# Optimization experiments

Hardware: AMD Instinct MI355X
Metric: run time of the kernel (lower is better)

## Reference

```python
import jax, jax.numpy as jnp
import numpy as np

EPS = 1e-6
RATIO = 0.5


def lrelu(x):
    return jnp.where(x > 0, x, 0.1 * x)


def conv1x1(x, w, b):
    # x (B,Ci,H,W), w (Co,Ci)
    return jnp.einsum('bihw,oi->bohw', x, w) + b[None, :, None, None]


def conv3x3(x, w, b, groups=1):
    y = jax.lax.conv_general_dilated(x, w, (1, 1), [(1, 1), (1, 1)],
        dimension_numbers=('NCHW', 'OIHW', 'NCHW'), feature_group_count=groups)
    return y + b[None, :, None, None]


def ln_cf(x, w, b):
    # channels-first LayerNorm over dim 1 (matches custom LayerNorm in source)
    u = x.mean(1, keepdims=True)
    s = ((x - u) ** 2).mean(1, keepdims=True)
    xn = (x - u) / jnp.sqrt(s + EPS)
    return w[None, :, None, None] * xn + b[None, :, None, None]


def flow_warp(x, flow):
    # bilinear warp, align_corners=True, zeros padding; flow (B,H,W,2): ch0=col offset, ch1=row offset (pixels)
    B, C, H, W = x.shape
    sx = jnp.arange(W, dtype=x.dtype)[None, None, :] + flow[..., 0]
    sy = jnp.arange(H, dtype=x.dtype)[None, :, None] + flow[..., 1]
    x0 = jnp.floor(sx)
    y0 = jnp.floor(sy)
    flat = x.reshape(B, C, H * W)

    def gather(xi, yi):
        valid = ((xi >= 0) & (xi <= W - 1) & (yi >= 0) & (yi <= H - 1)).astype(x.dtype)
        xc = jnp.clip(xi, 0, W - 1).astype(jnp.int32)
        yc = jnp.clip(yi, 0, H - 1).astype(jnp.int32)
        idx = (yc * W + xc).reshape(B, H * W)
        g = jnp.take_along_axis(flat, idx[:, None, :], axis=2).reshape(B, C, H, W)
        return g * valid[:, None, :, :]

    wx = sx - x0
    wy = sy - y0
    return (gather(x0, y0) * ((1 - wx) * (1 - wy))[:, None]
            + gather(x0 + 1, y0) * (wx * (1 - wy))[:, None]
            + gather(x0, y0 + 1) * ((1 - wx) * wy)[:, None]
            + gather(x0 + 1, y0 + 1) * (wx * wy)[:, None])


def mixer_forward(x, p_in_w, p_in_b, p_ln_w, p_ln_b, p_off_w1, p_off_b1, p_off_w2, p_off_b2,
                  p_ca_w, p_ca_b, p_sa_w, p_sa_b, p_mask_w1, p_mask_b1, p_mask_w2, p_mask_b2,
                  v_w, v_b, q_w, q_b, k_w, k_b, cs_w, cs_b, out_w, out_b):
    B, C, H, W = x.shape
    N = H * W
    # ---- Predictor (eval path) ----
    gy, gx = jnp.meshgrid(jnp.linspace(-1.0, 1.0, H), jnp.linspace(-1.0, 1.0, W), indexing='ij')
    grid = jnp.broadcast_to(jnp.stack([gx, gy]).astype(x.dtype)[None], (B, 2, H, W))
    cond = jnp.concatenate([x, grid], axis=1)  # (B, C+2, H, W)
    f = lrelu(ln_cf(conv1x1(cond, p_in_w, p_in_b), p_ln_w, p_ln_b))  # (B, (C+2)//4, H, W)
    offsets = jnp.tanh(conv1x1(lrelu(conv1x1(f, p_off_w1, p_off_b1)), p_off_w2, p_off_b2)) * 8.0
    ca = jax.nn.sigmoid(conv1x1(f.mean((2, 3), keepdims=True), p_ca_w, p_ca_b))  # (B,C,1,1)
    sa = jax.nn.sigmoid(conv3x3(f, p_sa_w, p_sa_b))  # (B,1,H,W)
    t = f.mean(1).reshape(B, N, 1)  # window_size=1 -> per-pixel token score input
    s1 = lrelu(t @ p_mask_w1.T + p_mask_b1)
    pred = jax.nn.softmax(s1 @ p_mask_w2.T + p_mask_b2, axis=-1)  # (B,N,2)
    score = pred[..., 0]
    num_keep = int(N * RATIO)  # static keep count (eval-mode deterministic routing)
    idx = jnp.argsort(-score, axis=1)
    idx1, idx2 = idx[:, :num_keep], idx[:, num_keep:]
    # ---- routed mixing ----
    v = conv1x1(x, v_w, v_b)
    k_img = x + flow_warp(x, offsets.transpose(0, 2, 3, 1))
    tok = lambda z: z.reshape(B, C, N).transpose(0, 2, 1)
    q_tok, k_tok, v_tok, vs_tok = tok(x), tok(k_img), tok(v), tok(v * sa)
    sel = lambda z, i: jnp.take_along_axis(z, i[..., None], axis=1)
    q1 = sel(q_tok, idx1) @ q_w.T + q_b
    k1 = sel(k_tok, idx1) @ k_w.T + k_b
    v1 = sel(v_tok, idx1)
    attn = jax.nn.softmax(jnp.einsum('bnc,bmc->bnm', q1, k1) * (C ** -0.5), axis=-1)
    f_attn = jnp.einsum('bnm,bmc->bnc', attn, v1)
    bi = jnp.arange(B)[:, None]
    out_tok = v_tok.at[bi, idx1].set(f_attn).at[bi, idx2].set(sel(vs_tok, idx2))  # batch_index_fill
    out = out_tok.transpose(0, 2, 1).reshape(B, C, H, W)
    out = jax.nn.gelu(conv3x3(out, cs_w, cs_b, groups=C)) * ca + out
    return conv1x1(out, out_w, out_b)


def setup_inputs():
    key = jax.random.key(0)
    ks = iter(jax.random.split(key, 40))
    B, C, H, W = 8, 192, 64, 64
    CD, C4, C8 = C + 2, (C + 2) // 4, (C + 2) // 8

    def w(shape, fan):
        return jax.random.normal(next(ks), shape, jnp.float32) * (fan ** -0.5)

    return dict(
        x=jax.random.normal(next(ks), (B, C, H, W), jnp.float32),
        p_in_w=w((C4, CD), CD), p_in_b=jnp.zeros((C4,)),
        p_ln_w=jnp.ones((C4,)), p_ln_b=jnp.zeros((C4,)),
        p_off_w1=w((C8, C4), C4), p_off_b1=jnp.zeros((C8,)),
        p_off_w2=w((2, C8), C8), p_off_b2=jnp.zeros((2,)),
        p_ca_w=w((C, C4), C4), p_ca_b=jnp.zeros((C,)),
        p_sa_w=w((1, C4, 3, 3), C4 * 9), p_sa_b=jnp.zeros((1,)),
        p_mask_w1=w((1, 1), 1), p_mask_b1=jnp.zeros((1,)),
        p_mask_w2=w((2, 1), 1), p_mask_b2=jnp.zeros((2,)),
        v_w=w((C, C), C), v_b=jnp.zeros((C,)),
        q_w=w((C, C), C), q_b=jnp.zeros((C,)),
        k_w=w((C, C), C), k_b=jnp.zeros((C,)),
        cs_w=w((C, 1, 3, 3), 9), cs_b=jnp.zeros((C,)),
        out_w=w((C, C), C), out_b=jnp.zeros((C,)),
    )


def reference(x, p_in_w, p_in_b, p_ln_w, p_ln_b, p_off_w1, p_off_b1, p_off_w2, p_off_b2,
              p_ca_w, p_ca_b, p_sa_w, p_sa_b, p_mask_w1, p_mask_b1, p_mask_w2, p_mask_b2,
              v_w, v_b, q_w, q_b, k_w, k_b, cs_w, cs_b, out_w, out_b):
    return mixer_forward(x, p_in_w, p_in_b, p_ln_w, p_ln_b, p_off_w1, p_off_b1, p_off_w2, p_off_b2,
                         p_ca_w, p_ca_b, p_sa_w, p_sa_b, p_mask_w1, p_mask_b1, p_mask_w2, p_mask_b2,
                         v_w, v_b, q_w, q_b, k_w, k_b, cs_w, cs_b, out_w, out_b)
```

## Files before the change

### kernel.cpp

```cpp
#include <hip/hip_runtime.h>
#include <hip/hip_bf16.h>

#define NB   8
#define NC   192
#define NH   64
#define NW   64
#define NN   4096
#define NCD  194
#define NC4  48
#define NKEEP 2048
#define NSPLIT 4
#define KPS   (NKEEP/NSPLIT)
#define NT    (KPS/32)

typedef __attribute__((ext_vector_type(8))) short bf16x8;
typedef __attribute__((ext_vector_type(4))) float f32x4;
typedef __hip_bfloat16 bf16;

__device__ __forceinline__ float dsigmoid(float x){ return 1.f/(1.f+__expf(-x)); }
__device__ __forceinline__ float dlrelu(float x){ return x>0.f ? x : 0.1f*x; }
__device__ __forceinline__ float b2f(short s){ return __uint_as_float(((unsigned)(unsigned short)s)<<16); }

__global__ __launch_bounds__(128) void k_f_score(
    const float* __restrict__ x, const float* __restrict__ w_in, const float* __restrict__ b_in,
    const float* __restrict__ ln_w, const float* __restrict__ ln_b,
    const float* __restrict__ mw1, const float* __restrict__ mb1,
    const float* __restrict__ mw2, const float* __restrict__ mb2,
    float* __restrict__ f, float* __restrict__ score)
{
  __shared__ float wT[NCD][NC4];
  int t = threadIdx.x;
  for (int i=t; i<NCD*NC4; i+=128){ int o = i/NCD, c = i - o*NCD; wT[c][o] = w_in[i]; }
  __syncthreads();

  int gid = blockIdx.x*128 + t;
  int p = gid & (NN-1), b = gid >> 12;
  int hh = p>>6, ww = p&63;

  f32x4 a4[12];
  #pragma unroll
  for (int j=0;j<12;++j) a4[j] = *(const f32x4*)(b_in + 4*j);

  const float* xb = x + (size_t)b*NC*NN + p;
  for (int c=0;c<NC;++c){
    float xv = xb[(size_t)c*NN];
    #pragma unroll
    for (int j=0;j<12;++j){ f32x4 wv = *(const f32x4*)&wT[c][4*j]; a4[j] += wv*xv; }
  }
  { float gx = -1.f + (2.f/63.f)*(float)ww;
    #pragma unroll
    for (int j=0;j<12;++j){ f32x4 wv = *(const f32x4*)&wT[192][4*j]; a4[j] += wv*gx; }
    float gy = -1.f + (2.f/63.f)*(float)hh;
    #pragma unroll
    for (int j=0;j<12;++j){ f32x4 wv = *(const f32x4*)&wT[193][4*j]; a4[j] += wv*gy; }
  }
  float s1=0.f, s2=0.f;
  #pragma unroll
  for (int j=0;j<12;++j){
    #pragma unroll
    for (int k=0;k<4;++k){ float v=a4[j][k]; s1+=v; s2+=v*v; }
  }
  float mean = s1*(1.f/NC4);
  float var  = s2*(1.f/NC4) - mean*mean;
  float rstd = rsqrtf(var + 1e-6f);
  float tsum = 0.f;
  #pragma unroll
  for (int j=0;j<12;++j){
    f32x4 lw = *(const f32x4*)(ln_w + 4*j);
    f32x4 lb = *(const f32x4*)(ln_b + 4*j);
    #pragma unroll
    for (int k=0;k<4;++k){
      float z = lw[k]*((a4[j][k]-mean)*rstd) + lb[k];
      float fv = z>0.f ? z : 0.1f*z;
      tsum += fv;
      f[((size_t)b*NC4 + 4*j+k)*NN + p] = fv;
    }
  }
  float tm = tsum*(1.f/NC4);
  float sv = dlrelu(tm*mw1[0] + mb1[0]);
  float d  = sv*(mw2[0]-mw2[1]) + (mb2[0]-mb2[1]);
  score[b*NN + p] = dsigmoid(d);
}

__global__ __launch_bounds__(1024) void k_topk(const float* __restrict__ score,
                                               int* __restrict__ idx1, int* __restrict__ flag)
{
  int b = blockIdx.x;
  int t = threadIdx.x;
  __shared__ unsigned hist[256];
  __shared__ unsigned long long sP;
  __shared__ unsigned sR;
  __shared__ unsigned cnt;
  unsigned long long key[4];
  #pragma unroll
  for (int j=0;j<4;++j){
    int i = t + j*1024;
    unsigned u = __float_as_uint(score[b*NN+i]);
    unsigned a = (u & 0x80000000u) ? ~u : (u | 0x80000000u);
    unsigned d = ~a;
    key[j] = ((unsigned long long)d << 32) | (unsigned)i;
  }
  if (t==0){ sP=0ull; sR=NKEEP-1; cnt=0u; }
  #pragma unroll 1
  for (int pass=0; pass<8; ++pass){
    int shift = 56 - pass*8;
    if (t<256) hist[t]=0u;
    __syncthreads();
    unsigned long long P = sP;
    #pragma unroll
    for (int j=0;j<4;++j){
      bool ok = (pass==0) || ((key[j] >> (shift+8)) == (P >> (shift+8)));
      if (ok) atomicAdd(&hist[(unsigned)((key[j]>>shift)&255ull)], 1u);
    }
    __syncthreads();
    if (t < 64){
      unsigned s[4]; unsigned lsum=0u;
      #pragma unroll
      for (int j=0;j<4;++j){ s[j]=hist[4*t+j]; lsum+=s[j]; }
      unsigned incl = lsum;
      #pragma unroll
      for (int d2=1; d2<64; d2<<=1){
        unsigned v = __shfl_up(incl, d2);
        if (t >= d2) incl += v;
      }
      unsigned before = incl - lsum;
      unsigned R = sR;
      if (R >= before && R < incl){
        unsigned c = before;
        #pragma unroll
        for (int j=0;j<4;++j){
          if (R < c + s[j]){
            sP = sP | ((unsigned long long)(4u*(unsigned)t + (unsigned)j) << shift);
            sR = R - c;
            break;
          }
          c += s[j];
        }
      }
    }
    __syncthreads();
  }
  unsigned long long P = sP;
  #pragma unroll
  for (int j=0;j<4;++j){
    int i = t + j*1024;
    bool sel = (key[j] <= P);
    flag[b*NN+i] = sel ? 1 : 0;
    if (sel){
      unsigned pos = atomicAdd(&cnt, 1u);
      idx1[b*NKEEP + pos] = i;
    }
  }
}

__global__ __launch_bounds__(256) void k_offsets(
    const float* __restrict__ f, const float* __restrict__ w1, const float* __restrict__ b1,
    const float* __restrict__ w2, const float* __restrict__ b2, float* __restrict__ offs)
{
  int gid = blockIdx.x*256 + threadIdx.x;
  int p = gid & (NN-1);
  int b = gid >> 12;
  const float* fb = f + (size_t)b*NC4*NN + p;
  float fl[NC4];
  #pragma unroll 8
  for (int c=0;c<NC4;++c) fl[c] = fb[(size_t)c*NN];
  float h1[24];
  for (int o=0;o<24;++o){
    const float* wr = w1 + o*NC4;
    float a = b1[o];
    #pragma unroll 8
    for (int c=0;c<NC4;++c) a += wr[c]*fl[c];
    h1[o] = dlrelu(a);
  }
  #pragma unroll
  for (int o=0;o<2;++o){
    const float* wr = w2 + o*24;
    float a = b2[o];
    #pragma unroll
    for (int c=0;c<24;++c) a += wr[c]*h1[c];
    offs[((size_t)b*2+o)*NN + p] = tanhf(a)*8.f;
  }
}

__global__ __launch_bounds__(256) void k_fmean(const float* __restrict__ f, float* __restrict__ fmean){
  int bc = blockIdx.x;
  const float* p = f + (size_t)bc*NN;
  float s = 0.f;
  for (int i=threadIdx.x;i<NN;i+=256) s += p[i];
  for (int o=32;o;o>>=1) s += __shfl_xor(s,o);
  __shared__ float r[4];
  if ((threadIdx.x&63)==0) r[threadIdx.x>>6] = s;
  __syncthreads();
  if (threadIdx.x==0) fmean[bc] = (r[0]+r[1]+r[2]+r[3])*(1.f/NN);
}

__global__ void k_ca(const float* __restrict__ fmean, const float* __restrict__ w,
                     const float* __restrict__ bias, float* __restrict__ ca){
  int b = blockIdx.x, o = threadIdx.x;
  const float* fm = fmean + b*NC4;
  float a = bias[o];
  #pragma unroll 8
  for (int c=0;c<NC4;++c) a += w[o*NC4+c]*fm[c];
  ca[b*NC+o] = dsigmoid(a);
}

__global__ __launch_bounds__(256) void k_sa(const float* __restrict__ f, const float* __restrict__ w,
                                            const float* __restrict__ bias, float* __restrict__ sa){
  int hh = blockIdx.x;
  int b  = blockIdx.y;
  __shared__ float fl[3][NC4][66];
  __shared__ float wl[NC4*9];
  __shared__ float ps[4][64];
  int t = threadIdx.x;

  for (int i=t; i<3*NC4*64; i+=256){
    int col = i & 63;
    int rc  = i >> 6;
    int cc  = rc % NC4;
    int rr  = rc / NC4;
    int yy  = hh + rr - 1;
    float v = (yy>=0 && yy<=63) ? f[((size_t)b*NC4+cc)*NN + yy*64 + col] : 0.f;
    fl[rr][cc][1+col] = v;
  }
  if (t < 3*NC4){ int rr=t/NC4, cc=t%NC4; fl[rr][cc][0]=0.f; fl[rr][cc][65]=0.f; }
  for (int i=t; i<NC4*9; i+=256) wl[i] = w[i];
  __syncthreads();

  int ww = t & 63, gq = t >> 6;
  float acc = 0.f;
  #pragma unroll
  for (int j=0;j<12;++j){
    int cc = gq*12 + j;
    const float* wc = &wl[cc*9];
    #pragma unroll
    for (int dy=0;dy<3;++dy){
      acc += fl[dy][cc][ww  ]*wc[dy*3+0];
      acc += fl[dy][cc][ww+1]*wc[dy*3+1];
      acc += fl[dy][cc][ww+2]*wc[dy*3+2];
    }
  }
  ps[gq][ww] = acc;
  __syncthreads();
  if (t < 64){
    float s = ps[0][t]+ps[1][t]+ps[2][t]+ps[3][t] + bias[0];
    sa[(size_t)b*NN + hh*64 + t] = dsigmoid(s);
  }
}

__global__ __launch_bounds__(256) void k_w2bf(const float* __restrict__ a, const float* __restrict__ b,
                                              const float* __restrict__ c, const float* __restrict__ d,
                                              bf16* __restrict__ oa, bf16* __restrict__ ob,
                                              bf16* __restrict__ oc, bf16* __restrict__ od){
  int i = blockIdx.x*256 + threadIdx.x;
  if (i < NC*NC){
    oa[i] = __float2bfloat16(a[i]);
    ob[i] = __float2bfloat16(b[i]);
    oc[i] = __float2bfloat16(c[i]);
    od[i] = __float2bfloat16(d[i]);
  }
}

__global__ __launch_bounds__(256) void k_transpose(const float* __restrict__ in, bf16* __restrict__ outT){
  int b = blockIdx.z;
  int c0 = blockIdx.y*32, p0 = blockIdx.x*32;
  __shared__ float tile[32][33];
  int col = threadIdx.x & 31, row8 = threadIdx.x >> 5;
  #pragma unroll
  for (int ph=0;ph<4;++ph){
    int c = c0 + ph*8 + row8;
    tile[ph*8+row8][col] = in[((size_t)b*NC + c)*NN + p0 + col];
  }
  __syncthreads();
  #pragma unroll
  for (int ph=0;ph<4;++ph){
    int p = p0 + ph*8 + row8;
    outT[((size_t)b*NN + p)*NC + c0 + col] = __float2bfloat16(tile[col][ph*8+row8]);
  }
}

__global__ __launch_bounds__(256) void k_conv_mfma(const bf16* __restrict__ inT, const bf16* __restrict__ wb,
                                                   const float* __restrict__ bias, float* __restrict__ outp){
  int b = blockIdx.y;
  int px0 = blockIdx.x*64;
  int wv = threadIdx.x>>6, lane = threadIdx.x&63, g = lane>>4, r = lane&15;
  int o0 = wv*48;
  bf16x8 bw[3][6];
  #pragma unroll
  for (int jo=0;jo<3;++jo)
    #pragma unroll
    for (int ks=0;ks<6;++ks)
      bw[jo][ks] = *(const bf16x8*)(wb + (size_t)(o0+jo*16+r)*NC + ks*32 + 8*g);
  float bv[3];
  #pragma unroll
  for (int jo=0;jo<3;++jo) bv[jo] = bias[o0+jo*16+r];

  const bf16* ib = inT + (size_t)b*NN*NC;
  #pragma unroll
  for (int t=0;t<4;++t){
    int px = px0 + t*16;
    bf16x8 a[6];
    #pragma unroll
    for (int ks=0;ks<6;++ks) a[ks] = *(const bf16x8*)(ib + (size_t)(px+r)*NC + ks*32 + 8*g);
    f32x4 acc[3];
    #pragma unroll
    for (int jo=0;jo<3;++jo){ acc[jo][0]=0.f; acc[jo][1]=0.f; acc[jo][2]=0.f; acc[jo][3]=0.f; }
    #pragma unroll
    for (int ks=0;ks<6;++ks)
      #pragma unroll
      for (int jo=0;jo<3;++jo)
        acc[jo] = __builtin_amdgcn_mfma_f32_16x16x32_bf16(a[ks], bw[jo][ks], acc[jo], 0,0,0);
    #pragma unroll
    for (int jo=0;jo<3;++jo){
      float4 rv; rv.x=acc[jo][0]+bv[jo]; rv.y=acc[jo][1]+bv[jo]; rv.z=acc[jo][2]+bv[jo]; rv.w=acc[jo][3]+bv[jo];
      *(float4*)(outp + ((size_t)b*NC + o0+jo*16+r)*NN + px + 4*g) = rv;
    }
  }
}

__global__ __launch_bounds__(256) void k_gemm_mfma(const bf16* __restrict__ in, const bf16* __restrict__ wb,
                                                   const float* __restrict__ bias, bf16* __restrict__ outp){
  int b = blockIdx.y;
  int s0 = blockIdx.x*32;
  int wv = threadIdx.x>>6, lane = threadIdx.x&63, g = lane>>4, r = lane&15;
  int o0 = wv*48;
  bf16x8 bw[3][6];
  #pragma unroll
  for (int jo=0;jo<3;++jo)
    #pragma unroll
    for (int ks=0;ks<6;++ks)
      bw[jo][ks] = *(const bf16x8*)(wb + (size_t)(o0+jo*16+r)*NC + ks*32 + 8*g);
  float bv[3];
  #pragma unroll
  for (int jo=0;jo<3;++jo) bv[jo] = bias[o0+jo*16+r];

  const bf16* ib = in + (size_t)b*NKEEP*NC;
  bf16* ob = outp + (size_t)b*NKEEP*NC;
  #pragma unroll
  for (int t=0;t<2;++t){
    int s = s0 + t*16;
    bf16x8 a[6];
    #pragma unroll
    for (int ks=0;ks<6;++ks) a[ks] = *(const bf16x8*)(ib + (size_t)(s+r)*NC + ks*32 + 8*g);
    f32x4 acc[3];
    #pragma unroll
    for (int jo=0;jo<3;++jo){ acc[jo][0]=0.f; acc[jo][1]=0.f; acc[jo][2]=0.f; acc[jo][3]=0.f; }
    #pragma unroll
    for (int ks=0;ks<6;++ks)
      #pragma unroll
      for (int jo=0;jo<3;++jo)
        acc[jo] = __builtin_amdgcn_mfma_f32_16x16x32_bf16(a[ks], bw[jo][ks], acc[jo], 0,0,0);
    #pragma unroll
    for (int jo=0;jo<3;++jo)
      #pragma unroll
      for (int i=0;i<4;++i)
        ob[(size_t)(s+4*g+i)*NC + o0+jo*16+r] = __float2bfloat16(acc[jo][i]+bv[jo]);
  }
}

__global__ __launch_bounds__(256) void k_warp_params(const int* __restrict__ idx1, const float* __restrict__ offs,
                                                     float4* __restrict__ wpar, int4* __restrict__ ipar){
  int gid = blockIdx.x*256 + threadIdx.x;
  int b = gid >> 11;
  int p = idx1[gid];
  int ph = p >> 6, pwx = p & 63;
  float fx = offs[((size_t)b*2+0)*NN + p];
  float fy = offs[((size_t)b*2+1)*NN + p];
  float sx = (float)pwx + fx, sy = (float)ph + fy;
  float x0f = floorf(sx), y0f = floorf(sy);
  float wx = sx - x0f, wy = sy - y0f;
  int x0 = (int)x0f, y0 = (int)y0f;
  bool vx0 = (x0f >= 0.f) && (x0f <= 63.f);
  bool vx1 = (x0f+1.f >= 0.f) && (x0f+1.f <= 63.f);
  bool vy0 = (y0f >= 0.f) && (y0f <= 63.f);
  bool vy1 = (y0f+1.f >= 0.f) && (y0f+1.f <= 63.f);
  int cx0 = min(max(x0,0),63), cx1 = min(max(x0+1,0),63);
  int cy0 = min(max(y0,0),63), cy1 = min(max(y0+1,0),63);
  float4 w4;
  w4.x = (vx0&&vy0) ? (1.f-wx)*(1.f-wy) : 0.f;
  w4.y = (vx1&&vy0) ? wx*(1.f-wy)       : 0.f;
  w4.z = (vx0&&vy1) ? (1.f-wx)*wy       : 0.f;
  w4.w = (vx1&&vy1) ? wx*wy             : 0.f;
  int4 i4;
  i4.x = cy0*64+cx0; i4.y = cy0*64+cx1; i4.z = cy1*64+cx0; i4.w = cy1*64+cx1;
  wpar[gid]=w4; ipar[gid]=i4;
}

__global__ __launch_bounds__(256) void k_gather_qT(const bf16* __restrict__ xT, const int* __restrict__ idx1,
                                                   bf16* __restrict__ qin){
  int gid = blockIdx.x*256 + threadIdx.x;
  int j = gid % 24;
  int bs = gid / 24;
  int b = bs >> 11;
  int p = idx1[bs];
  *(bf16x8*)(qin + (size_t)bs*NC + j*8) = *(const bf16x8*)(xT + ((size_t)b*NN + p)*NC + j*8);
}

__global__ __launch_bounds__(256) void k_gather_kT(const bf16* __restrict__ xT, const int* __restrict__ idx1,
                                                   const float4* __restrict__ wpar, const int4* __restrict__ ipar,
                                                   bf16* __restrict__ kin){
  int gid = blockIdx.x*256 + threadIdx.x;
  int j = gid % 24;
  int bs = gid / 24;
  int b = bs >> 11;
  int p = idx1[bs];
  float4 w4 = wpar[bs]; int4 i4 = ipar[bs];
  const bf16* xb = xT + (size_t)b*NN*NC + j*8;
  bf16x8 v0 = *(const bf16x8*)(xb + (size_t)p*NC);
  bf16x8 v1 = *(const bf16x8*)(xb + (size_t)i4.x*NC);
  bf16x8 v2 = *(const bf16x8*)(xb + (size_t)i4.y*NC);
  bf16x8 v3 = *(const bf16x8*)(xb + (size_t)i4.z*NC);
  bf16x8 v4 = *(const bf16x8*)(xb + (size_t)i4.w*NC);
  bf16x8 o;
  #pragma unroll
  for (int k=0;k<8;++k){
    float vv = b2f(v0[k]) + w4.x*b2f(v1[k]) + w4.y*b2f(v2[k]) + w4.z*b2f(v3[k]) + w4.w*b2f(v4[k]);
    bf16 h = __float2bfloat16(vv);
    o[k] = *(short*)&h;
  }
  *(bf16x8*)(kin + (size_t)bs*NC + j*8) = o;
}

__global__ __launch_bounds__(256) void k_gather_vT(const float* __restrict__ v, const int* __restrict__ idx1,
                                                   bf16* __restrict__ v1T){
  int gid = blockIdx.x*256 + threadIdx.x;
  int s = gid & (NKEEP-1);
  int bc = gid >> 11;
  int b = bc/NC;
  v1T[gid] = __float2bfloat16(v[(size_t)bc*NN + idx1[b*NKEEP+s]]);
}

__global__ __launch_bounds__(256) void k_fill(const float* __restrict__ sa, const int* __restrict__ flag,
                                              float* __restrict__ vout){
  int gid = blockIdx.x*256 + threadIdx.x;
  int p = gid & (NN-1);
  int bc = gid >> 12;
  int b = bc/NC;
  if (!flag[b*NN+p]) vout[gid] *= sa[b*NN+p];
}

__global__ __launch_bounds__(256) void k_attn(const bf16* __restrict__ q1, const bf16* __restrict__ k1,
                                              const bf16* __restrict__ v1T,
                                              bf16* __restrict__ pacc, float* __restrict__ pl)
{
  int b = blockIdx.y, qb = blockIdx.x, sp = blockIdx.z;
  int tid = threadIdx.x;
  int wv = tid >> 6;
  int lane = tid & 63;
  int g = lane >> 4, r = lane & 15;
  int q0 = qb*64 + wv*16;

  const bf16* qbp = q1 + (size_t)b*NKEEP*NC;
  const char* kgb = (const char*)(k1 + (size_t)b*NKEEP*NC);
  const char* vgb = (const char*)(v1T + (size_t)b*NC*NKEEP);

  __shared__ __align__(1024) char kl[12288];
  __shared__ __align__(1024) char vl[2][12288];
  __shared__ __align__(16) bf16 plds[4][16][40];
  bf16 (* __restrict__ pw)[40] = plds[wv];
  char* klc = kl;

  int ksrc[3], vsrc[3];
  #pragma unroll
  for (int i=0;i<3;++i){
    int j = wv*3 + i;
    int o = j*1024 + lane*16;
    int rr = o/384, cb = o - rr*384;
    ksrc[i] = rr*384 + (cb ^ ((rr&7)<<4));
    int ch = o>>6, kb2 = o&63;
    vsrc[i] = ch*(NKEEP*2) + kb2;
  }

  const int kbase = sp*KPS;
  auto stage = [&](int k0, int vb){
    char* vlc = vl[vb];
    #pragma unroll
    for (int i=0;i<3;++i){
      int j = wv*3 + i;
      __builtin_amdgcn_global_load_lds(
        (const __attribute__((address_space(1))) void*)(kgb + (size_t)k0*384 + ksrc[i]),
        (__attribute__((address_space(3))) void*)(klc + j*1024), 16, 0, 0);
      __builtin_amdgcn_global_load_lds(
        (const __attribute__((address_space(1))) void*)(vgb + (size_t)k0*2 + vsrc[i]),
        (__attribute__((address_space(3))) void*)(vlc + j*1024), 16, 0, 0);
    }
  };

  bf16x8 aq[6];
  #pragma unroll
  for (int ks=0;ks<6;++ks)
    aq[ks] = *(const bf16x8*)(qbp + (size_t)(q0+r)*NC + 32*ks + 8*g);

  f32x4 acc[12];
  #pragma unroll
  for (int i=0;i<12;++i){ acc[i][0]=0.f; acc[i][1]=0.f; acc[i][2]=0.f; acc[i][3]=0.f; }
  float l[4]={0.f,0.f,0.f,0.f};

  const float scale = 0.07216878364870323f;
  const float shift = 20.f;
  const int swz = (r&7)<<4;

  stage(kbase, 0);
  __syncthreads();

  int vb = 0;
  for (int t16=0;t16<NT;++t16) {
    f32x4 s0v, s1v;
    s0v[0]=s0v[1]=s0v[2]=s0v[3]=0.f;
    s1v[0]=s1v[1]=s1v[2]=s1v[3]=0.f;
    #pragma unroll
    for (int ks=0;ks<6;++ks) {
      int co = (ks*64 + g*16) ^ swz;
      bf16x8 bk0 = *(const bf16x8*)(klc + r*384 + co);
      bf16x8 bk1 = *(const bf16x8*)(klc + (16+r)*384 + co);
      s0v = __builtin_amdgcn_mfma_f32_16x16x32_bf16(aq[ks], bk0, s0v, 0,0,0);
      s1v = __builtin_amdgcn_mfma_f32_16x16x32_bf16(aq[ks], bk1, s1v, 0,0,0);
    }
    #pragma unroll
    for (int i=0;i<4;++i) {
      float e0 = __expf(s0v[i]*scale - shift);
      float e1 = __expf(s1v[i]*scale - shift);
      l[i] += e0 + e1;
      pw[4*g+i][r]    = __float2bfloat16(e0);
      pw[4*g+i][16+r] = __float2bfloat16(e1);
    }
    bf16x8 pa = *(const bf16x8*)(&pw[r][8*g]);

    __syncthreads();
    if (t16+1 < NT) stage(kbase + (t16+1)*32, vb^1);

    const char* vlc = vl[vb];
    #pragma unroll
    for (int ct=0;ct<12;++ct) {
      bf16x8 bvv = *(const bf16x8*)(vlc + (16*ct + r)*64 + g*16);
      acc[ct] = __builtin_amdgcn_mfma_f32_16x16x32_bf16(pa, bvv, acc[ct], 0,0,0);
    }
    __syncthreads();
    vb ^= 1;
  }

  #pragma unroll
  for (int i=0;i<4;++i){
    #pragma unroll
    for (int o=1;o<16;o<<=1) l[i] += __shfl_xor(l[i],o);
  }
  size_t pbase = (((size_t)(b*32+qb)*NSPLIT + sp)*64);
  if (r==0){
    #pragma unroll
    for (int i=0;i<4;++i) pl[pbase + wv*16 + 4*g + i] = l[i];
  }
  #pragma unroll
  for (int ct=0;ct<12;++ct)
    #pragma unroll
    for (int i=0;i<4;++i)
      pacc[(pbase + wv*16 + 4*g + i)*NC + 16*ct + r] = __float2bfloat16(acc[ct][i]);
}

__global__ __launch_bounds__(256) void k_merge(const bf16* __restrict__ pacc,
                                               const float* __restrict__ pl, const int* __restrict__ idx1,
                                               float* __restrict__ out_img)
{
  int gid = blockIdx.x*256 + threadIdx.x;
  int c = gid % NC;
  int bs = gid / NC;
  int s = bs & (NKEEP-1);
  int b = bs >> 11;
  int qb = s >> 6, ql = s & 63;
  size_t base = ((size_t)(b*32+qb)*NSPLIT)*64 + ql;
  float l = pl[base] + pl[base+64] + pl[base+128] + pl[base+192];
  size_t pb = base*NC + c;
  float v = __bfloat162float(pacc[pb])
          + __bfloat162float(pacc[pb + (size_t)64*NC])
          + __bfloat162float(pacc[pb + (size_t)128*NC])
          + __bfloat162float(pacc[pb + (size_t)192*NC]);
  out_img[((size_t)b*NC + c)*NN + idx1[b*NKEEP + s]] = v / l;
}

__global__ __launch_bounds__(256) void k_dwgelu(const float* __restrict__ vin, const float* __restrict__ ca,
                                                const float* __restrict__ cw, const float* __restrict__ cb,
                                                float* __restrict__ out2){
  int bc = blockIdx.x;
  int c = bc % NC, b = bc / NC;
  __shared__ float tl[66][66];
  int t = threadIdx.x;

  if (t < 66){ tl[0][t] = 0.f; tl[65][t] = 0.f; }
  if (t < 64){ tl[t+1][0] = 0.f; tl[t+1][65] = 0.f; }
  const float* ip = vin + (size_t)bc*NN;
  #pragma unroll
  for (int k=0;k<4;++k){
    int p4 = (t + k*256)*4;
    int hh = p4 >> 6, ww = p4 & 63;
    float4 v4 = *(const float4*)(ip + p4);
    tl[1+hh][1+ww  ] = v4.x;
    tl[1+hh][1+ww+1] = v4.y;
    tl[1+hh][1+ww+2] = v4.z;
    tl[1+hh][1+ww+3] = v4.w;
  }
  float wr[9];
  #pragma unroll
  for (int i=0;i<9;++i) wr[i] = cw[c*9+i];
  float cbv = cb[c];
  float cav = ca[b*NC+c];
  __syncthreads();

  float* op = out2 + (size_t)bc*NN;
  #pragma unroll
  for (int k=0;k<16;++k){
    int p = t + k*256;
    int hh = p >> 6, ww = p & 63;
    float a = cbv;
    #pragma unroll
    for (int dy=0;dy<3;++dy){
      a += tl[hh+dy][ww  ]*wr[dy*3+0];
      a += tl[hh+dy][ww+1]*wr[dy*3+1];
      a += tl[hh+dy][ww+2]*wr[dy*3+2];
    }
    float gl = 0.5f*a*(1.f+tanhf(0.79788456080286536f*(a+0.044715f*a*a*a)));
    op[p] = gl*cav + tl[1+hh][1+ww];
  }
}

extern "C" void kernel_launch(void* const* d_in, const int* in_sizes, int n_in,
                              void* d_out, int out_size, void* d_ws, size_t ws_size,
                              hipStream_t stream)
{
  const float* x       = (const float*)d_in[0];
  const float* p_in_w  = (const float*)d_in[1];
  const float* p_in_b  = (const float*)d_in[2];
  const float* p_ln_w  = (const float*)d_in[3];
  const float* p_ln_b  = (const float*)d_in[4];
  const float* p_off_w1= (const float*)d_in[5];
  const float* p_off_b1= (const float*)d_in[6];
  const float* p_off_w2= (const float*)d_in[7];
  const float* p_off_b2= (const float*)d_in[8];
  const float* p_ca_w  = (const float*)d_in[9];
  const float* p_ca_b  = (const float*)d_in[10];
  const float* p_sa_w  = (const float*)d_in[11];
  const float* p_sa_b  = (const float*)d_in[12];
  const float* p_mask_w1=(const float*)d_in[13];
  const float* p_mask_b1=(const float*)d_in[14];
  const float* p_mask_w2=(const float*)d_in[15];
  const float* p_mask_b2=(const float*)d_in[16];
  const float* v_w     = (const float*)d_in[17];
  const float* v_b     = (const float*)d_in[18];
  const float* q_w     = (const float*)d_in[19];
  const float* q_b     = (const float*)d_in[20];
  const float* k_w     = (const float*)d_in[21];
  const float* k_b     = (const float*)d_in[22];
  const float* cs_w    = (const float*)d_in[23];
  const float* cs_b    = (const float*)d_in[24];
  const float* out_w   = (const float*)d_in[25];
  const float* out_b   = (const float*)d_in[26];
  float* out = (float*)d_out;
  (void)in_sizes; (void)n_in; (void)out_size;

  char* wsp = (char*)d_ws;
  size_t off = 0;
  auto alloc = [&](size_t bytes)->char*{ char* p = wsp + off; off += (bytes + 255) & ~(size_t)255; return p; };
  float* f     = (float*)alloc((size_t)NB*NC4*NN*4);
  float* score = (float*)alloc((size_t)NB*NN*4);
  int*   idx1  = (int*)  alloc((size_t)NB*NKEEP*4);
  int*   flag  = (int*)  alloc((size_t)NB*NN*4);
  float* offs  = (float*)alloc((size_t)NB*2*NN*4);
  float* sa    = (float*)alloc((size_t)NB*NN*4);
  float* fmean = (float*)alloc((size_t)NB*NC4*4);
  float* ca    = (float*)alloc((size_t)NB*NC*4);
  float* vbuf  = (float*)alloc((size_t)NB*NC*NN*4);
  bf16*  q1bf  = (bf16*) alloc((size_t)NB*NKEEP*NC*2);
  bf16*  k1bf  = (bf16*) alloc((size_t)NB*NKEEP*NC*2);
  bf16*  v1T   = (bf16*) alloc((size_t)NB*NC*NKEEP*2);
  float4* wpar = (float4*)alloc((size_t)NB*NKEEP*16);
  int4*   ipar = (int4*) alloc((size_t)NB*NKEEP*16);
  float* out2  = (float*)alloc((size_t)NB*NC*NN*4);
  float* pl    = (float*)alloc((size_t)NB*32*NSPLIT*64*4);
  bf16*  xT    = (bf16*) alloc((size_t)NB*NN*NC*2);
  bf16*  wqb   = (bf16*) alloc((size_t)NC*NC*2);
  bf16*  wkb   = (bf16*) alloc((size_t)NC*NC*2);
  bf16*  wvb   = (bf16*) alloc((size_t)NC*NC*2);
  bf16*  wob   = (bf16*) alloc((size_t)NC*NC*2);
  if (off > ws_size) return;
  bf16* qin  = (bf16*)out2;
  bf16* kin  = qin + (size_t)NB*NKEEP*NC;
  bf16* pacc = (bf16*)out2;
  bf16* out2T = xT;

  k_w2bf<<<(NC*NC+255)/256, 256, 0, stream>>>(q_w, k_w, v_w, out_w, wqb, wkb, wvb, wob);
  k_transpose<<<dim3(NN/32, NC/32, NB), 256, 0, stream>>>(x, xT);
  k_f_score<<<NB*NN/128, 128, 0, stream>>>(x, p_in_w, p_in_b, p_ln_w, p_ln_b,
      p_mask_w1, p_mask_b1, p_mask_w2, p_mask_b2, f, score);
  k_topk<<<NB, 1024, 0, stream>>>(score, idx1, flag);
  k_offsets<<<NB*NN/256, 256, 0, stream>>>(f, p_off_w1, p_off_b1, p_off_w2, p_off_b2, offs);
  k_fmean<<<NB*NC4, 256, 0, stream>>>(f, fmean);
  k_ca<<<NB, NC, 0, stream>>>(fmean, p_ca_w, p_ca_b, ca);
  k_sa<<<dim3(NH, NB), 256, 0, stream>>>(f, p_sa_w, p_sa_b, sa);
  k_conv_mfma<<<dim3(NN/64, NB), 256, 0, stream>>>(xT, wvb, v_b, vbuf);
  k_warp_params<<<NB*NKEEP/256, 256, 0, stream>>>(idx1, offs, wpar, ipar);
  k_gather_qT<<<NB*NKEEP*24/256, 256, 0, stream>>>(xT, idx1, qin);
  k_gather_kT<<<NB*NKEEP*24/256, 256, 0, stream>>>(xT, idx1, wpar, ipar, kin);
  k_gemm_mfma<<<dim3(NKEEP/32, NB), 256, 0, stream>>>(qin, wqb, q_b, q1bf);
  k_gemm_mfma<<<dim3(NKEEP/32, NB), 256, 0, stream>>>(kin, wkb, k_b, k1bf);
  k_gather_vT<<<NB*NC*NKEEP/256, 256, 0, stream>>>(vbuf, idx1, v1T);
  k_fill<<<NB*NC*NN/256, 256, 0, stream>>>(sa, flag, vbuf);
  k_attn<<<dim3(NKEEP/64, NB, NSPLIT), 256, 0, stream>>>(q1bf, k1bf, v1T, pacc, pl);
  k_merge<<<NB*NKEEP*NC/256, 256, 0, stream>>>(pacc, pl, idx1, vbuf);
  k_dwgelu<<<NB*NC, 256, 0, stream>>>(vbuf, ca, cs_w, cs_b, out2);
  k_transpose<<<dim3(NN/32, NC/32, NB), 256, 0, stream>>>(out2, out2T);
  k_conv_mfma<<<dim3(NN/64, NB), 256, 0, stream>>>(out2T, wob, out_b, out);
}
```

Measured before the change: 433.2 us.

## Fuse saliency fill into value conv, halve attention splits, relayout K/V LDS tiles

The separate k_fill pass over the full value tensor is removed. Its per-pixel saliency scaling now runs in the epilogue of the value 1x1 conv, which saves a full read-modify-write of the value tensor. The attention split count drops from 4 to 2, so less partial output is written and k_merge reduces fewer partials, at the cost of fewer, longer attention blocks. K and V tiles in LDS are relaid out in 16-byte octet-major order instead of an XOR swizzle, and block indices are linearised with batch in the low bits.

```diff
diff --git a/kernel.cpp b/kernel.cpp
--- a/kernel.cpp
+++ b/kernel.cpp
@@ -9,7 +9,7 @@
 #define NCD  194
 #define NC4  48
 #define NKEEP 2048
-#define NSPLIT 4
+#define NSPLIT 2
 #define KPS   (NKEEP/NSPLIT)
 #define NT    (KPS/32)
 
@@ -279,7 +279,8 @@
 }
 
 __global__ __launch_bounds__(256) void k_conv_mfma(const bf16* __restrict__ inT, const bf16* __restrict__ wb,
-                                                   const float* __restrict__ bias, float* __restrict__ outp){
+                                                   const float* __restrict__ bias, float* __restrict__ outp,
+                                                   const int* __restrict__ flag, const float* __restrict__ sa){
   int b = blockIdx.y;
   int px0 = blockIdx.x*64;
   int wv = threadIdx.x>>6, lane = threadIdx.x&63, g = lane>>4, r = lane&15;
@@ -309,9 +310,21 @@
       #pragma unroll
       for (int jo=0;jo<3;++jo)
         acc[jo] = __builtin_amdgcn_mfma_f32_16x16x32_bf16(a[ks], bw[jo][ks], acc[jo], 0,0,0);
+    float m0=1.f, m1=1.f, m2=1.f, m3=1.f;
+    if (flag){
+      int pix = px + 4*g;
+      int4 f4 = *(const int4*)(flag + (size_t)b*NN + pix);
+      float4 s4 = *(const float4*)(sa + (size_t)b*NN + pix);
+      m0 = f4.x ? 1.f : s4.x;
+      m1 = f4.y ? 1.f : s4.y;
+      m2 = f4.z ? 1.f : s4.z;
+      m3 = f4.w ? 1.f : s4.w;
+    }
     #pragma unroll
     for (int jo=0;jo<3;++jo){
-      float4 rv; rv.x=acc[jo][0]+bv[jo]; rv.y=acc[jo][1]+bv[jo]; rv.z=acc[jo][2]+bv[jo]; rv.w=acc[jo][3]+bv[jo];
+      float4 rv;
+      rv.x=(acc[jo][0]+bv[jo])*m0; rv.y=(acc[jo][1]+bv[jo])*m1;
+      rv.z=(acc[jo][2]+bv[jo])*m2; rv.w=(acc[jo][3]+bv[jo])*m3;
       *(float4*)(outp + ((size_t)b*NC + o0+jo*16+r)*NN + px + 4*g) = rv;
     }
   }
@@ -429,20 +442,15 @@
   v1T[gid] = __float2bfloat16(v[(size_t)bc*NN + idx1[b*NKEEP+s]]);
 }
 
-__global__ __launch_bounds__(256) void k_fill(const float* __restrict__ sa, const int* __restrict__ flag,
-                                              float* __restrict__ vout){
-  int gid = blockIdx.x*256 + threadIdx.x;
-  int p = gid & (NN-1);
-  int bc = gid >> 12;
-  int b = bc/NC;
-  if (!flag[b*NN+p]) vout[gid] *= sa[b*NN+p];
-}
-
 __global__ __launch_bounds__(256) void k_attn(const bf16* __restrict__ q1, const bf16* __restrict__ k1,
                                               const bf16* __restrict__ v1T,
                                               bf16* __restrict__ pacc, float* __restrict__ pl)
 {
-  int b = blockIdx.y, qb = blockIdx.x, sp = blockIdx.z;
+  int id = blockIdx.x;
+  int b  = id & 7;
+  int t2 = id >> 3;
+  int sp = t2 & (NSPLIT-1);
+  int qb = t2 >> 1;
   int tid = threadIdx.x;
   int wv = tid >> 6;
   int lane = tid & 63;
@@ -462,12 +470,13 @@
   int ksrc[3], vsrc[3];
   #pragma unroll
   for (int i=0;i<3;++i){
-    int j = wv*3 + i;
-    int o = j*1024 + lane*16;
-    int rr = o/384, cb = o - rr*384;
-    ksrc[i] = rr*384 + (cb ^ ((rr&7)<<4));
-    int ch = o>>6, kb2 = o&63;
-    vsrc[i] = ch*(NKEEP*2) + kb2;
+    int o = (wv*3 + i)*1024 + lane*16;
+    int koct = o >> 9;
+    int krow = (o >> 4) & 31;
+    ksrc[i] = krow*384 + koct*16;
+    int voct = o / 3072;
+    int vch  = (o - voct*3072) >> 4;
+    vsrc[i] = vch*(NKEEP*2) + voct*16;
   }
 
   const int kbase = sp*KPS;
@@ -497,7 +506,6 @@
 
   const float scale = 0.07216878364870323f;
   const float shift = 20.f;
-  const int swz = (r&7)<<4;
 
   stage(kbase, 0);
   __syncthreads();
@@ -509,9 +517,9 @@
     s1v[0]=s1v[1]=s1v[2]=s1v[3]=0.f;
     #pragma unroll
     for (int ks=0;ks<6;++ks) {
-      int co = (ks*64 + g*16) ^ swz;
-      bf16x8 bk0 = *(const bf16x8*)(klc + r*384 + co);
-      bf16x8 bk1 = *(const bf16x8*)(klc + (16+r)*384 + co);
+      const char* kp = klc + (size_t)(4*ks+g)*512 + r*16;
+      bf16x8 bk0 = *(const bf16x8*)(kp);
+      bf16x8 bk1 = *(const bf16x8*)(kp + 256);
       s0v = __builtin_amdgcn_mfma_f32_16x16x32_bf16(aq[ks], bk0, s0v, 0,0,0);
       s1v = __builtin_amdgcn_mfma_f32_16x16x32_bf16(aq[ks], bk1, s1v, 0,0,0);
     }
@@ -531,7 +539,7 @@
     const char* vlc = vl[vb];
     #pragma unroll
     for (int ct=0;ct<12;++ct) {
-      bf16x8 bvv = *(const bf16x8*)(vlc + (16*ct + r)*64 + g*16);
+      bf16x8 bvv = *(const bf16x8*)(vlc + g*3072 + (16*ct + r)*16);
       acc[ct] = __builtin_amdgcn_mfma_f32_16x16x32_bf16(pa, bvv, acc[ct], 0,0,0);
     }
     __syncthreads();
@@ -566,12 +574,10 @@
   int b = bs >> 11;
   int qb = s >> 6, ql = s & 63;
   size_t base = ((size_t)(b*32+qb)*NSPLIT)*64 + ql;
-  float l = pl[base] + pl[base+64] + pl[base+128] + pl[base+192];
+  float l = pl[base] + pl[base+64];
   size_t pb = base*NC + c;
   float v = __bfloat162float(pacc[pb])
-          + __bfloat162float(pacc[pb + (size_t)64*NC])
-          + __bfloat162float(pacc[pb + (size_t)128*NC])
-          + __bfloat162float(pacc[pb + (size_t)192*NC]);
+          + __bfloat162float(pacc[pb + (size_t)64*NC]);
   out_img[((size_t)b*NC + c)*NN + idx1[b*NKEEP + s]] = v / l;
 }
 
@@ -693,17 +699,16 @@
   k_fmean<<<NB*NC4, 256, 0, stream>>>(f, fmean);
   k_ca<<<NB, NC, 0, stream>>>(fmean, p_ca_w, p_ca_b, ca);
   k_sa<<<dim3(NH, NB), 256, 0, stream>>>(f, p_sa_w, p_sa_b, sa);
-  k_conv_mfma<<<dim3(NN/64, NB), 256, 0, stream>>>(xT, wvb, v_b, vbuf);
+  k_conv_mfma<<<dim3(NN/64, NB), 256, 0, stream>>>(xT, wvb, v_b, vbuf, flag, sa);
   k_warp_params<<<NB*NKEEP/256, 256, 0, stream>>>(idx1, offs, wpar, ipar);
   k_gather_qT<<<NB*NKEEP*24/256, 256, 0, stream>>>(xT, idx1, qin);
   k_gather_kT<<<NB*NKEEP*24/256, 256, 0, stream>>>(xT, idx1, wpar, ipar, kin);
   k_gemm_mfma<<<dim3(NKEEP/32, NB), 256, 0, stream>>>(qin, wqb, q_b, q1bf);
   k_gemm_mfma<<<dim3(NKEEP/32, NB), 256, 0, stream>>>(kin, wkb, k_b, k1bf);
   k_gather_vT<<<NB*NC*NKEEP/256, 256, 0, stream>>>(vbuf, idx1, v1T);
-  k_fill<<<NB*NC*NN/256, 256, 0, stream>>>(sa, flag, vbuf);
-  k_attn<<<dim3(NKEEP/64, NB, NSPLIT), 256, 0, stream>>>(q1bf, k1bf, v1T, pacc, pl);
+  k_attn<<<NB*NSPLIT*32, 256, 0, stream>>>(q1bf, k1bf, v1T, pacc, pl);
   k_merge<<<NB*NKEEP*NC/256, 256, 0, stream>>>(pacc, pl, idx1, vbuf);
   k_dwgelu<<<NB*NC, 256, 0, stream>>>(vbuf, ca, cs_w, cs_b, out2);
   k_transpose<<<dim3(NN/32, NC/32, NB), 256, 0, stream>>>(out2, out2T);
-  k_conv_mfma<<<dim3(NN/64, NB), 256, 0, stream>>>(out2T, wob, out_b, out);
-}
+  k_conv_mfma<<<dim3(NN/64, NB), 256, 0, stream>>>(out2T, wob, out_b, out, nullptr, nullptr);
+}
```

After: 426.8 us. Within noise of the previous version (-1.5%).
